# Kernel optimization log

Hardware: AMD Instinct MI355X
Metric: run time of the kernel (lower is better)

Reference implementation:

```python
import jax, jax.numpy as jnp
import numpy as np

INF = 1e10
EPS = 1e-5
B, N, F, H, NC, NRBF = 2, 512, 64, 64, 32, 50
GAMMA = 10.0  # RBF width for the continuous filter convolution kernel


def setup_inputs() -> dict:
    key = jax.random.key(0)
    ks = jax.random.split(key, 16)
    def lin(k, i, o):
        return (jax.random.normal(k, (i, o), jnp.float32) / np.sqrt(i)).astype(jnp.float32)
    d = {}
    d["h"] = jax.random.normal(ks[0], (B, N, F), jnp.float32)
    d["x"] = jax.random.normal(ks[1], (B, N, 3), jnp.float32)
    d["mask"] = jnp.ones((B, N, N), jnp.float32)
    # ContinuousFilterConvolution(2F -> H): feature branch + RBF filter branch
    d["W_dh"] = lin(ks[2], 2 * F, H); d["b_dh"] = jnp.zeros((H,), jnp.float32)
    d["mu"] = jnp.linspace(0.0, 5.0, NRBF).astype(jnp.float32)
    d["W_f"] = lin(ks[3], NRBF, H); d["b_f"] = jnp.zeros((H,), jnp.float32)
    # semantic_attention_mlp: Linear(2F,1,bias=False) + SiLU
    d["W_sa"] = lin(ks[4], 2 * F, 1)
    # edge_weight_mlp: Linear(2F+H, NC) + Tanh
    d["W_ew"] = lin(ks[5], 2 * F + H, NC); d["b_ew"] = jnp.zeros((NC,), jnp.float32)
    # post_norm_nlp: Linear(NC,H) SiLU Linear(H,H)
    d["W_pn1"] = lin(ks[6], NC, H); d["b_pn1"] = jnp.zeros((H,), jnp.float32)
    d["W_pn2"] = lin(ks[7], H, H); d["b_pn2"] = jnp.zeros((H,), jnp.float32)
    # node_mlp: Linear(2H+F,H) SiLU Linear(H,H)
    d["W_nm1"] = lin(ks[8], 2 * H + F, H); d["b_nm1"] = jnp.zeros((H,), jnp.float32)
    d["W_nm2"] = lin(ks[9], H, H); d["b_nm2"] = jnp.zeros((H,), jnp.float32)
    # coordinate_mlp: Linear(H,H) SiLU Linear(H,1)
    d["W_cm1"] = lin(ks[10], H, H); d["b_cm1"] = jnp.zeros((H,), jnp.float32)
    d["W_cm2"] = lin(ks[11], H, 1); d["b_cm2"] = jnp.zeros((1,), jnp.float32)
    return d


def reference(h, x, mask, W_dh, b_dh, mu, W_f, b_f, W_sa, W_ew, b_ew,
              W_pn1, b_pn1, W_pn2, b_pn2, W_nm1, b_nm1, W_nm2, b_nm2,
              W_cm1, b_cm1, W_cm2, b_cm2):
    silu = jax.nn.silu
    n = h.shape[-2]
    # pairwise displacements: entry [b,i,j] = x[b,j] - x[b,i]
    x_minus_xt = x[..., None, :, :] - x[..., :, None, :]                       # [B,N,N,3]
    norm = jnp.sqrt(jax.nn.relu(jnp.sum(x_minus_xt ** 2, -1, keepdims=True)) + EPS)  # [B,N,N,1]
    eye = jnp.eye(n, dtype=norm.dtype)[..., None]                              # [N,N,1]
    _norm = norm + INF * eye + (1.0 - mask[..., None]) * INF
    spatial = jax.nn.softmax(-_norm, axis=-2)                                  # softmin over senders
    # h_cat_ht[b,i,j] = concat(h[b,j], h[b,i])
    hi = jnp.broadcast_to(h[..., None, :, :], h.shape[:-2] + (n, n, h.shape[-1]))
    hj = jnp.broadcast_to(h[..., :, None, :], h.shape[:-2] + (n, n, h.shape[-1]))
    h_cat = jnp.concatenate([hi, hj], -1)                                      # [B,N,N,2F]
    # continuous filter convolution: feature MLP gated by RBF-expanded distance filter
    rbf = jnp.exp(-GAMMA * (norm - mu) ** 2)                                   # [B,N,N,NRBF]
    filtered = (h_cat @ W_dh + b_dh) * (rbf @ W_f + b_f)                       # [B,N,N,H]
    # semantic attention
    sem = silu(h_cat @ W_sa)                                                   # [B,N,N,1]
    sem = sem - INF * eye + (mask[..., None] - 1.0) * INF
    sem = jax.nn.softmax(sem, axis=-2)
    # per-edge coefficient weights on normalized displacement vectors
    w = jnp.tanh(jnp.concatenate([h_cat, filtered], -1) @ W_ew + b_ew)         # [B,N,N,NC]
    dirvec = x_minus_xt / (norm ** 2 + EPS)                                    # [B,N,N,3]
    att = w[..., None] * dirvec[..., None, :] * mask[..., None, None]          # [B,N,N,NC,3]
    att_sum = att.sum(-3)                                                      # sum over j -> [B,N,NC,3]
    att_norm = jnp.sqrt(jax.nn.relu(jnp.sum(att_sum ** 2, -1)) + EPS)          # [B,N,NC]
    emb = silu(att_norm @ W_pn1 + b_pn1) @ W_pn2 + b_pn2                       # [B,N,H]
    # edge messages and coordinate update
    h_e = filtered * mask[..., None]
    _h_e = (silu(h_e @ W_cm1 + b_cm1) @ W_cm2 + b_cm2) * mask[..., None]       # [B,N,N,1]
    _x = (x_minus_xt * _h_e).sum(-2) + x                                       # [B,N,3]
    # combined spatial*semantic attention and aggregation
    total = jax.nn.softmax(sem * spatial + (mask[..., None] - 1.0) * INF, axis=-2)
    h_e_agg = (total * h_e).sum(-2)                                            # [B,N,H]
    z = jnp.concatenate([h, h_e_agg, emb], -1)                                 # [B,N,F+2H]
    _h = silu(z @ W_nm1 + b_nm1) @ W_nm2 + b_nm2                               # [B,N,H]
    return _h, _x
```

## Files before the change

### kernel.cpp

```cpp
#include <hip/hip_runtime.h>

#define INF 1e10f
#define EPSV 1e-5f
#define NB 2
#define NN 512
#define NF 64
#define NH 64
#define NCC 32
#define NRBF 50
#define NND (NB*NN)
#define MU_STEP (5.0f/49.0f)

typedef _Float16 half8 __attribute__((ext_vector_type(8)));
typedef float f32x4 __attribute__((ext_vector_type(4)));

__device__ __forceinline__ float frcp(float x){ return __builtin_amdgcn_rcpf(x); }
__device__ __forceinline__ float silu_f(float x){ return x * frcp(1.f + __expf(-x)); }
__device__ __forceinline__ float tanh_f(float x){
  float t = __expf(2.f * x);
  return fmaf(-2.f, frcp(t + 1.f), 1.f);
}

__device__ __forceinline__ float wredSum(float v){
  v += __shfl_down(v, 32); v += __shfl_down(v, 16); v += __shfl_down(v, 8);
  v += __shfl_down(v, 4);  v += __shfl_down(v, 2);  v += __shfl_down(v, 1);
  return v;
}
__device__ __forceinline__ float bredSum(float v, float* red, int tid){
  float w = wredSum(v);
  __syncthreads();
  if ((tid & 63) == 0) red[tid >> 6] = w;
  __syncthreads();
  return (red[0] + red[1]) + (red[2] + red[3]);
}
__device__ __forceinline__ float2 bredSum2(float a, float b, float* red, int tid){
  float wa = wredSum(a), wb = wredSum(b);
  __syncthreads();
  if ((tid & 63) == 0){ red[(tid >> 6) * 2] = wa; red[(tid >> 6) * 2 + 1] = wb; }
  __syncthreads();
  return make_float2(red[0] + red[2] + red[4] + red[6],
                     red[1] + red[3] + red[5] + red[7]);
}

__global__ void kA(const float* __restrict__ h, const float* __restrict__ Wdh,
                   const float* __restrict__ Wew, const float* __restrict__ Wsa,
                   const float* __restrict__ bdh, const float* __restrict__ bew,
                   const float* __restrict__ Wf, const float* __restrict__ bf,
                   const float* __restrict__ Wcm1,
                   float* __restrict__ u, float* __restrict__ vb,
                   float* __restrict__ e1r, float* __restrict__ e2c,
                   float* __restrict__ s1, float* __restrict__ s2,
                   unsigned int* __restrict__ frag){
  const int tid = threadIdx.x;
  const int sub = tid >> 6, l = tid & 63;
  const int node = blockIdx.x * 4 + sub;
  __shared__ float sh[4][NF];
  sh[sub][l] = h[node * NF + l];
  __syncthreads();
  float ua = 0.f, va = 0.f;
  #pragma unroll
  for (int f = 0; f < NF; ++f){
    float hv = sh[sub][f];
    ua = fmaf(hv, Wdh[f * NH + l], ua);
    va = fmaf(hv, Wdh[(NF + f) * NH + l], va);
  }
  u[node * NH + l] = ua;
  vb[node * NH + l] = va + bdh[l];
  const int nc = l & 31;
  const int half = l >> 5;
  float ea = 0.f;
  #pragma unroll
  for (int f = 0; f < NF; ++f) ea = fmaf(sh[sub][f], Wew[(half * NF + f) * NCC + nc], ea);
  if (half == 0) e1r[node * NCC + nc] = ea;
  else           e2c[node * NCC + nc] = ea + bew[nc];
  if (l < 2){
    const float* wp = Wsa + l * NF;
    float s = 0.f;
    #pragma unroll
    for (int f = 0; f < NF; ++f) s = fmaf(sh[sub][f], wp[f], s);
    if (l == 0) s1[node] = s; else s2[node] = s;
  }
  if (blockIdx.x < 20){
    const int fi = blockIdx.x;
    const int lane = tid >> 2, dw = tid & 3;
    float v[2];
    #pragma unroll
    for (int e2 = 0; e2 < 2; ++e2){
      int e = dw * 2 + e2;
      int kk = 8 * (lane >> 4) + e;
      int n16 = lane & 15;
      float val;
      if (fi < 8){
        int mt = fi >> 1, kc = fi & 1;
        int hh = 8 * (n16 >> 2) + (n16 & 3) + 4 * (mt & 1) + 32 * (mt >> 1);
        int r = kk + 32 * kc;
        val = (r < NRBF) ? Wf[r * NH + hh] : ((r == NRBF) ? bf[hh] : 0.f);
      } else if (fi < 16){
        int q = fi - 8; int kc = q >> 2, nt = q & 3;
        val = Wcm1[(kk + 32 * kc) * NH + (n16 + 16 * nt)];
      } else {
        int q = fi - 16; int kc = q >> 1, n2 = q & 1;
        val = Wew[(2 * NF + kk + 32 * kc) * NCC + (n16 + 16 * n2)];
      }
      v[e2] = val;
    }
    unsigned int lo = (unsigned int)__builtin_bit_cast(unsigned short, (_Float16)v[0]);
    unsigned int hi = (unsigned int)__builtin_bit_cast(unsigned short, (_Float16)v[1]);
    frag[fi * 256 + lane * 4 + dw] = lo | (hi << 16);
  }
}

__global__ __launch_bounds__(256, 2) void kB(
    const float* __restrict__ x, const float* __restrict__ mask,
    const float* __restrict__ h_g,
    const float* __restrict__ u, const float* __restrict__ vb,
    const float* __restrict__ s1g, const float* __restrict__ s2g,
    const float* __restrict__ e1r, const float* __restrict__ e2c,
    const float* __restrict__ Wc2, const float* __restrict__ bc1, const float* __restrict__ bc2g,
    const unsigned int* __restrict__ frag,
    const float* __restrict__ Wpn1, const float* __restrict__ bpn1,
    const float* __restrict__ Wpn2, const float* __restrict__ bpn2,
    const float* __restrict__ Wnm1, const float* __restrict__ bnm1,
    const float* __restrict__ Wnm2, const float* __restrict__ bnm2,
    float* __restrict__ out)
{
  const int bid = blockIdx.x;
  const int b = bid >> 9, i = bid & (NN - 1);
  const int tid = threadIdx.x;
  const int lane = tid & 63, wave = tid >> 6;
  const int l15 = lane & 15, g = lane >> 4;
  const int base = b * NN;

  __shared__ __align__(16) float4 s_geo[NN];
  __shared__ __align__(16) float4 s_c[NN];
  __shared__ float s_m[NN];
  __shared__ float s_red[8];
  __shared__ half8 s_WB[20][64];

  {
    const int4* src = (const int4*)frag;
    int4* dst = (int4*)&s_WB[0][0];
    #pragma unroll
    for (int q = 0; q < 5; ++q) dst[tid + q * 256] = src[tid + q * 256];
  }

  const float xi0 = x[(base + i) * 3 + 0];
  const float xi1 = x[(base + i) * 3 + 1];
  const float xi2 = x[(base + i) * 3 + 2];
  const float s2i = s2g[base + i];

  float ea[2], es[2], mj[2];
  #pragma unroll
  for (int q = 0; q < 2; ++q){
    const int j = tid + q * 256;
    float d0 = x[(base + j) * 3 + 0] - xi0;
    float d1 = x[(base + j) * 3 + 1] - xi1;
    float d2 = x[(base + j) * 3 + 2] - xi2;
    float nsq = d0 * d0 + d1 * d1 + d2 * d2;
    float norm = sqrtf(fmaxf(nsq, 0.f) + EPSV);
    float m = mask[(base + i) * NN + j];
    float eye = (j == i) ? 1.f : 0.f;
    ea[q] = __expf(-(norm + eye * INF + (1.f - m) * INF));
    float sp = s1g[base + j] + s2i;
    es[q] = __expf(silu_f(sp) - eye * INF + (m - 1.f) * INF);
    s_geo[j] = make_float4(d0, d1, d2, norm);
    s_m[j] = m;
    float inv = frcp(norm * norm + EPSV) * m;
    s_c[j] = make_float4(d0 * inv, d1 * inv, d2 * inv, 0.f);
    mj[q] = m;
  }
  float2 S12 = bredSum2(ea[0] + ea[1], es[0] + es[1], s_red, tid);
  const float iS1 = 1.f / S12.x, iS2 = 1.f / S12.y;
  float e3[2];
  #pragma unroll
  for (int q = 0; q < 2; ++q)
    e3[q] = __expf((es[q] * iS2) * (ea[q] * iS1) + (mj[q] - 1.f) * INF);
  float S3 = bredSum(e3[0] + e3[1], s_red, tid);
  const float iS3 = 1.f / S3;
  s_c[tid].w       = e3[0] * iS3 * mj[0];
  s_c[tid + 256].w = e3[1] * iS3 * mj[1];
  __syncthreads();

  float vba[16];
  {
    const float4* vp = (const float4*)(vb + (size_t)(base + i) * NH);
    float4 a0 = vp[2*g], a1 = vp[2*g+1], a2 = vp[2*g+8], a3 = vp[2*g+9];
    vba[0]=a0.x; vba[1]=a0.y; vba[2]=a0.z; vba[3]=a0.w;
    vba[4]=a1.x; vba[5]=a1.y; vba[6]=a1.z; vba[7]=a1.w;
    vba[8]=a2.x; vba[9]=a2.y; vba[10]=a2.z; vba[11]=a2.w;
    vba[12]=a3.x; vba[13]=a3.y; vba[14]=a3.z; vba[15]=a3.w;
  }
  float wc2v[4], bc1v[4];
  #pragma unroll
  for (int nt = 0; nt < 4; ++nt){ wc2v[nt] = Wc2[l15 + 16*nt]; bc1v[nt] = bc1[l15 + 16*nt]; }
  float e2v[2];
  e2v[0] = e2c[(size_t)(base + i) * NCC + l15];
  e2v[1] = e2c[(size_t)(base + i) * NCC + l15 + 16];
  const float bc2v16 = bc2g[0] * 0.0625f;
  const float mub0 = (float)(8 * g) * MU_STEP;
  const float mub1 = (float)(8 * g + 32) * MU_STEP;

  float hg[16];
  #pragma unroll
  for (int e = 0; e < 16; ++e) hg[e] = 0.f;
  float at[2][3] = {{0.f,0.f,0.f},{0.f,0.f,0.f}};
  float xa0 = 0.f, xa1 = 0.f, xa2 = 0.f;

  float4 u0, u1, u2, u3;
  {
    const float4* up = (const float4*)(u + (size_t)(base + wave*128 + l15) * NH);
    u0 = up[2*g]; u1 = up[2*g+1]; u2 = up[2*g+8]; u3 = up[2*g+9];
  }
  float e1v[4][2];
  #pragma unroll
  for (int reg = 0; reg < 4; ++reg){
    const float* ep1 = e1r + (size_t)(base + wave*128 + 4*g + reg) * NCC + l15;
    e1v[reg][0] = ep1[0]; e1v[reg][1] = ep1[16];
  }

  for (int jt8 = 0; jt8 < 8; ++jt8){
    const int jt = wave * 128 + jt8 * 16;
    const int jl = jt + l15;
    float normj = s_geo[jl].w;
    float tmw = s_c[jl].w;
    half8 brb[2];
    {
      float t0 = normj - mub0, t1 = normj - mub1;
      #pragma unroll
      for (int rr = 0; rr < 8; ++rr){
        float d0 = t0 - (float)rr * MU_STEP;
        float d1 = t1 - (float)rr * MU_STEP;
        float ev0 = __expf(-10.f * d0 * d0);
        float ev1 = __expf(-10.f * d1 * d1);
        int r1 = 8*g + rr + 32;
        brb[0][rr] = (_Float16)ev0;
        brb[1][rr] = (_Float16)((r1 < NRBF) ? ev1 : ((r1 == NRBF) ? 1.f : 0.f));
      }
    }
    f32x4 fc[4];
    __builtin_amdgcn_s_setprio(1);
    #pragma unroll
    for (int mt = 0; mt < 4; ++mt){
      f32x4 z = {0.f,0.f,0.f,0.f};
      z = __builtin_amdgcn_mfma_f32_16x16x32_f16(s_WB[2*mt][lane],   brb[0], z, 0, 0, 0);
      z = __builtin_amdgcn_mfma_f32_16x16x32_f16(s_WB[2*mt+1][lane], brb[1], z, 0, 0, 0);
      fc[mt] = z;
    }
    __builtin_amdgcn_s_setprio(0);
    float ua[16] = {u0.x,u0.y,u0.z,u0.w, u1.x,u1.y,u1.z,u1.w,
                    u2.x,u2.y,u2.z,u2.w, u3.x,u3.y,u3.z,u3.w};
    float FH[16];
    half8 afh[2];
    #pragma unroll
    for (int kc = 0; kc < 2; ++kc)
      #pragma unroll
      for (int e = 0; e < 8; ++e){
        int el = kc*8 + e;
        float f = fc[2*kc + (e>>2)][e & 3];
        FH[el] = (ua[el] + vba[el]) * f;
        afh[kc][e] = (_Float16)FH[el];
      }
    {
      const int jn = (jt8 < 7) ? (jl + 16) : jl;
      const float4* upn = (const float4*)(u + (size_t)(base + jn) * NH);
      u0 = upn[2*g]; u1 = upn[2*g+1]; u2 = upn[2*g+8]; u3 = upn[2*g+9];
    }
    #pragma unroll
    for (int e = 0; e < 16; ++e) hg[e] = fmaf(tmw, FH[e], hg[e]);
    f32x4 cm[4];
    f32x4 ew[2];
    __builtin_amdgcn_s_setprio(1);
    #pragma unroll
    for (int nt = 0; nt < 4; ++nt){
      f32x4 z = {0.f,0.f,0.f,0.f};
      z = __builtin_amdgcn_mfma_f32_16x16x32_f16(afh[0], s_WB[8+nt][lane],  z, 0, 0, 0);
      z = __builtin_amdgcn_mfma_f32_16x16x32_f16(afh[1], s_WB[12+nt][lane], z, 0, 0, 0);
      cm[nt] = z;
    }
    #pragma unroll
    for (int n2 = 0; n2 < 2; ++n2){
      f32x4 z = {0.f,0.f,0.f,0.f};
      z = __builtin_amdgcn_mfma_f32_16x16x32_f16(afh[0], s_WB[16+n2][lane], z, 0, 0, 0);
      z = __builtin_amdgcn_mfma_f32_16x16x32_f16(afh[1], s_WB[18+n2][lane], z, 0, 0, 0);
      ew[n2] = z;
    }
    __builtin_amdgcn_s_setprio(0);
    float mreg[4]; float4 geo4[4], c4[4];
    #pragma unroll
    for (int reg = 0; reg < 4; ++reg){
      int jr = jt + 4*g + reg;
      mreg[reg] = s_m[jr];
      geo4[reg] = s_geo[jr];
      c4[reg]   = s_c[jr];
    }
    float hEp[4] = {0.f,0.f,0.f,0.f};
    #pragma unroll
    for (int nt = 0; nt < 4; ++nt)
      #pragma unroll
      for (int reg = 0; reg < 4; ++reg){
        float tv = silu_f(fmaf(mreg[reg], cm[nt][reg], bc1v[nt]));
        hEp[reg] = fmaf(tv, wc2v[nt], hEp[reg]);
      }
    #pragma unroll
    for (int reg = 0; reg < 4; ++reg){
      float gm = mreg[reg];
      float hv = hEp[reg] + bc2v16;
      xa0 = fmaf(geo4[reg].x * gm, hv, xa0);
      xa1 = fmaf(geo4[reg].y * gm, hv, xa1);
      xa2 = fmaf(geo4[reg].z * gm, hv, xa2);
    }
    #pragma unroll
    for (int n2 = 0; n2 < 2; ++n2)
      #pragma unroll
      for (int reg = 0; reg < 4; ++reg){
        float wv = tanh_f(ew[n2][reg] + e1v[reg][n2] + e2v[n2]);
        at[n2][0] = fmaf(wv, c4[reg].x, at[n2][0]);
        at[n2][1] = fmaf(wv, c4[reg].y, at[n2][1]);
        at[n2][2] = fmaf(wv, c4[reg].z, at[n2][2]);
      }
    {
      const int jtn = jt + ((jt8 < 7) ? 16 : 0);
      #pragma unroll
      for (int reg = 0; reg < 4; ++reg){
        const float* ep1 = e1r + (size_t)(base + jtn + 4*g + reg) * NCC + l15;
        e1v[reg][0] = ep1[0]; e1v[reg][1] = ep1[16];
      }
    }
  }

  #pragma unroll
  for (int e = 0; e < 16; ++e){
    float v = hg[e];
    v += __shfl_xor(v, 1); v += __shfl_xor(v, 2);
    v += __shfl_xor(v, 4); v += __shfl_xor(v, 8);
    hg[e] = v;
  }
  #pragma unroll
  for (int n2 = 0; n2 < 2; ++n2)
    #pragma unroll
    for (int d = 0; d < 3; ++d){
      float v = at[n2][d];
      v += __shfl_xor(v, 16); v += __shfl_xor(v, 32);
      at[n2][d] = v;
    }
  #pragma unroll
  for (int s = 1; s <= 32; s <<= 1){
    xa0 += __shfl_xor(xa0, s);
    xa1 += __shfl_xor(xa1, s);
    xa2 += __shfl_xor(xa2, s);
  }

  __syncthreads();
  float* ep = (float*)&s_WB[0][0];
  if (l15 == 0){
    #pragma unroll
    for (int e = 0; e < 16; ++e)
      ep[wave*64 + 8*g + (e & 7) + 32*(e >> 3)] = hg[e];
  }
  if (lane < 16){
    #pragma unroll
    for (int n2 = 0; n2 < 2; ++n2)
      #pragma unroll
      for (int d = 0; d < 3; ++d)
        ep[256 + wave*96 + (l15 + 16*n2)*3 + d] = at[n2][d];
  }
  if (lane == 0){
    ep[640 + wave*3 + 0] = xa0; ep[640 + wave*3 + 1] = xa1; ep[640 + wave*3 + 2] = xa2;
  }
  __syncthreads();
  if (tid < 64)
    ep[832 + tid] = ep[tid] + ep[64+tid] + ep[128+tid] + ep[192+tid];
  if (tid >= 64 && tid < 160){
    int t = tid - 64;
    ep[704 + t] = ep[256+t] + ep[352+t] + ep[448+t] + ep[544+t];
  }
  if (tid >= 192 && tid < 195){
    int d = tid - 192;
    out[NB*NN*NH + (base + i)*3 + d] =
        ep[640+d] + ep[643+d] + ep[646+d] + ep[649+d] + x[(base + i)*3 + d];
  }
  __syncthreads();
  if (tid < 32){
    float a0 = ep[704 + tid*3], a1 = ep[704 + tid*3 + 1], a2 = ep[704 + tid*3 + 2];
    ep[896 + tid] = sqrtf(fmaxf(a0*a0 + a1*a1 + a2*a2, 0.f) + EPSV);
  }
  __syncthreads();

  if (wave == 0){
    const int k = lane;
    const int node = base + i;
    ep[1056 + k] = h_g[node * NF + k];
    asm volatile("s_waitcnt lgkmcnt(0)" ::: "memory");
    __builtin_amdgcn_wave_barrier();
    float acc = bpn1[k];
    #pragma unroll
    for (int t = 0; t < NCC; ++t) acc = fmaf(ep[896 + t], Wpn1[t * NH + k], acc);
    ep[928 + k] = silu_f(acc);
    asm volatile("s_waitcnt lgkmcnt(0)" ::: "memory");
    __builtin_amdgcn_wave_barrier();
    acc = bpn2[k];
    #pragma unroll
    for (int t = 0; t < NH; ++t) acc = fmaf(ep[928 + t], Wpn2[t * NH + k], acc);
    ep[992 + k] = acc;
    asm volatile("s_waitcnt lgkmcnt(0)" ::: "memory");
    __builtin_amdgcn_wave_barrier();
    acc = bnm1[k];
    #pragma unroll
    for (int t = 0; t < NF; ++t) acc = fmaf(ep[1056 + t], Wnm1[t * NH + k], acc);
    #pragma unroll
    for (int t = 0; t < NH; ++t) acc = fmaf(ep[832 + t],  Wnm1[(NF + t) * NH + k], acc);
    #pragma unroll
    for (int t = 0; t < NH; ++t) acc = fmaf(ep[992 + t],  Wnm1[(NF + NH + t) * NH + k], acc);
    float srv = silu_f(acc);
    asm volatile("s_waitcnt lgkmcnt(0)" ::: "memory");
    __builtin_amdgcn_wave_barrier();
    ep[928 + k] = srv;
    asm volatile("s_waitcnt lgkmcnt(0)" ::: "memory");
    __builtin_amdgcn_wave_barrier();
    acc = bnm2[k];
    #pragma unroll
    for (int t = 0; t < NH; ++t) acc = fmaf(ep[928 + t], Wnm2[t * NH + k], acc);
    out[node * NH + k] = acc;
  }
}

extern "C" void kernel_launch(void* const* d_in, const int* in_sizes, int n_in,
                              void* d_out, int out_size, void* d_ws, size_t ws_size,
                              hipStream_t stream){
  const float* h    = (const float*)d_in[0];
  const float* x    = (const float*)d_in[1];
  const float* mask = (const float*)d_in[2];
  const float* Wdh  = (const float*)d_in[3];
  const float* bdh  = (const float*)d_in[4];
  const float* Wf   = (const float*)d_in[6];
  const float* bf   = (const float*)d_in[7];
  const float* Wsa  = (const float*)d_in[8];
  const float* Wew  = (const float*)d_in[9];
  const float* bew  = (const float*)d_in[10];
  const float* Wpn1 = (const float*)d_in[11];
  const float* bpn1 = (const float*)d_in[12];
  const float* Wpn2 = (const float*)d_in[13];
  const float* bpn2 = (const float*)d_in[14];
  const float* Wnm1 = (const float*)d_in[15];
  const float* bnm1 = (const float*)d_in[16];
  const float* Wnm2 = (const float*)d_in[17];
  const float* bnm2 = (const float*)d_in[18];
  const float* Wcm1 = (const float*)d_in[19];
  const float* bcm1 = (const float*)d_in[20];
  const float* Wcm2 = (const float*)d_in[21];
  const float* bcm2 = (const float*)d_in[22];
  float* out = (float*)d_out;
  float* ws  = (float*)d_ws;

  float* u    = ws;
  float* vbuf = u    + 65536;
  float* s1   = vbuf + 65536;
  float* s2   = s1   + 1024;
  float* e1r  = s2   + 1024;
  float* e2c  = e1r  + 32768;
  unsigned int* fragb = (unsigned int*)(e2c + 32768);

  hipLaunchKernelGGL(kA, dim3(NND / 4), dim3(256), 0, stream,
                     h, Wdh, Wew, Wsa, bdh, bew, Wf, bf, Wcm1,
                     u, vbuf, e1r, e2c, s1, s2, fragb);
  hipLaunchKernelGGL(kB, dim3(NND), dim3(256), 0, stream,
                     x, mask, h, u, vbuf, s1, s2, e1r, e2c,
                     Wcm2, bcm1, bcm2, fragb,
                     Wpn1, bpn1, Wpn2, bpn2, Wnm1, bnm1, Wnm2, bnm2, out);
}
```

Before: 54.47 us.

## Compute RBF Gaussians by recurrence, premask geometry, load e1 per iteration

Measured after the change: 53.20 us (median of 2 runs). 1.02x faster.

```diff
diff --git a/kernel.cpp b/kernel.cpp
--- a/kernel.cpp
+++ b/kernel.cpp
@@ -10,6 +10,7 @@
 #define NRBF 50
 #define NND (NB*NN)
 #define MU_STEP (5.0f/49.0f)
+#define C20S (20.f*MU_STEP)
 
 typedef _Float16 half8 __attribute__((ext_vector_type(8)));
 typedef float f32x4 __attribute__((ext_vector_type(4)));
@@ -163,7 +164,7 @@
     ea[q] = __expf(-(norm + eye * INF + (1.f - m) * INF));
     float sp = s1g[base + j] + s2i;
     es[q] = __expf(silu_f(sp) - eye * INF + (m - 1.f) * INF);
-    s_geo[j] = make_float4(d0, d1, d2, norm);
+    s_geo[j] = make_float4(d0 * m, d1 * m, d2 * m, norm);
     s_m[j] = m;
     float inv = frcp(norm * norm + EPSV) * m;
     s_c[j] = make_float4(d0 * inv, d1 * inv, d2 * inv, 0.f);
@@ -199,6 +200,9 @@
   const float bc2v16 = bc2g[0] * 0.0625f;
   const float mub0 = (float)(8 * g) * MU_STEP;
   const float mub1 = (float)(8 * g + 32) * MU_STEP;
+  const float QCONST = __expf(-20.f * MU_STEP * MU_STEP);
+  const float crho0 = -10.f * MU_STEP * MU_STEP * (float)(16 * g + 1);
+  const float crho1 = -10.f * MU_STEP * MU_STEP * (float)(16 * g + 65);
 
   float hg[16];
   #pragma unroll
@@ -210,12 +214,6 @@
   {
     const float4* up = (const float4*)(u + (size_t)(base + wave*128 + l15) * NH);
     u0 = up[2*g]; u1 = up[2*g+1]; u2 = up[2*g+8]; u3 = up[2*g+9];
-  }
-  float e1v[4][2];
-  #pragma unroll
-  for (int reg = 0; reg < 4; ++reg){
-    const float* ep1 = e1r + (size_t)(base + wave*128 + 4*g + reg) * NCC + l15;
-    e1v[reg][0] = ep1[0]; e1v[reg][1] = ep1[16];
   }
 
   for (int jt8 = 0; jt8 < 8; ++jt8){
@@ -225,16 +223,22 @@
     float tmw = s_c[jl].w;
     half8 brb[2];
     {
-      float t0 = normj - mub0, t1 = normj - mub1;
+      float d0 = normj - mub0;
+      float d1 = normj - mub1;
+      float e0 = __expf(-10.f * d0 * d0);
+      float e1 = __expf(-10.f * d1 * d1);
+      float r0a = __expf(fmaf(C20S, normj, crho0));
+      float r1a = __expf(fmaf(C20S, normj, crho1));
+      const int rbase1 = 8*g + 32;
+      brb[0][0] = (_Float16)e0;
+      brb[1][0] = (_Float16)((rbase1 < NRBF) ? e1 : ((rbase1 == NRBF) ? 1.f : 0.f));
       #pragma unroll
-      for (int rr = 0; rr < 8; ++rr){
-        float d0 = t0 - (float)rr * MU_STEP;
-        float d1 = t1 - (float)rr * MU_STEP;
-        float ev0 = __expf(-10.f * d0 * d0);
-        float ev1 = __expf(-10.f * d1 * d1);
-        int r1 = 8*g + rr + 32;
-        brb[0][rr] = (_Float16)ev0;
-        brb[1][rr] = (_Float16)((r1 < NRBF) ? ev1 : ((r1 == NRBF) ? 1.f : 0.f));
+      for (int rr = 1; rr < 8; ++rr){
+        e0 *= r0a;  r0a *= QCONST;
+        e1 *= r1a;  r1a *= QCONST;
+        int r1i = rbase1 + rr;
+        brb[0][rr] = (_Float16)e0;
+        brb[1][rr] = (_Float16)((r1i < NRBF) ? e1 : ((r1i == NRBF) ? 1.f : 0.f));
       }
     }
     f32x4 fc[4];
@@ -267,6 +271,12 @@
     }
     #pragma unroll
     for (int e = 0; e < 16; ++e) hg[e] = fmaf(tmw, FH[e], hg[e]);
+    float e1v[4][2];
+    #pragma unroll
+    for (int reg = 0; reg < 4; ++reg){
+      const float* ep1 = e1r + (size_t)(base + jt + 4*g + reg) * NCC + l15;
+      e1v[reg][0] = ep1[0]; e1v[reg][1] = ep1[16];
+    }
     f32x4 cm[4];
     f32x4 ew[2];
     __builtin_amdgcn_s_setprio(1);
@@ -303,11 +313,10 @@
       }
     #pragma unroll
     for (int reg = 0; reg < 4; ++reg){
-      float gm = mreg[reg];
       float hv = hEp[reg] + bc2v16;
-      xa0 = fmaf(geo4[reg].x * gm, hv, xa0);
-      xa1 = fmaf(geo4[reg].y * gm, hv, xa1);
-      xa2 = fmaf(geo4[reg].z * gm, hv, xa2);
+      xa0 = fmaf(geo4[reg].x, hv, xa0);
+      xa1 = fmaf(geo4[reg].y, hv, xa1);
+      xa2 = fmaf(geo4[reg].z, hv, xa2);
     }
     #pragma unroll
     for (int n2 = 0; n2 < 2; ++n2)
@@ -318,14 +327,6 @@
         at[n2][1] = fmaf(wv, c4[reg].y, at[n2][1]);
         at[n2][2] = fmaf(wv, c4[reg].z, at[n2][2]);
       }
-    {
-      const int jtn = jt + ((jt8 < 7) ? 16 : 0);
-      #pragma unroll
-      for (int reg = 0; reg < 4; ++reg){
-        const float* ep1 = e1r + (size_t)(base + jtn + 4*g + reg) * NCC + l15;
-        e1v[reg][0] = ep1[0]; e1v[reg][1] = ep1[16];
-      }
-    }
   }
 
   #pragma unroll
```
